# Kernel optimization log

Measured on AMD Instinct MI355X. Metric: run time of the kernel, lower is better.

## Reference

```python
import jax, jax.numpy as jnp
import numpy as np

EPS = 1e-08
TOP_K_PERCENT = 0.3


def _stft_mag(x, n_fft, hop):
    # torch.stft defaults: center=True (reflect pad n_fft//2), window=None (rect), onesided
    pad = n_fft // 2
    xp = jnp.pad(x, ((0, 0), (pad, pad)), mode='reflect')
    n_frames = 1 + (xp.shape[-1] - n_fft) // hop
    idx = jnp.arange(n_frames)[:, None] * hop + jnp.arange(n_fft)[None, :]
    frames = xp[:, idx]                       # [B, T, n_fft]
    spec = jnp.fft.rfft(frames, axis=-1)      # [B, T, F]
    mag = jnp.abs(spec).swapaxes(-1, -2)      # [B, F, T]
    return jnp.maximum(mag, EPS)


def _patchify(m, ps):
    # same patch partition as torch unfold/unfold/reshape (within-patch element
    # order differs but only per-patch means are consumed)
    B, F, T = m.shape
    pf = (-F) % ps
    pt = (-T) % ps
    mp = jnp.pad(m, ((0, 0), (0, pf), (0, pt)))
    nF, nT = (F + pf) // ps, (T + pt) // ps
    return mp.reshape(B, nF, ps, nT, ps).transpose(0, 1, 3, 2, 4).reshape(B, nF * nT, ps * ps)


def setup_inputs() -> dict:
    key = jax.random.key(0)
    ks, kt, kg = jax.random.split(key, 3)
    B, L = 16, 262144
    return {
        'student_waveform': jax.random.normal(ks, (B, L), dtype=jnp.float32),
        'teacher_waveform': jax.random.normal(kt, (B, L), dtype=jnp.float32),
        'target_waveform': jax.random.normal(kg, (B, L), dtype=jnp.float32),
        'n_fft': 1024,
        'hop_length': 256,
        'patch_size': 16,
    }


def reference(student_waveform, teacher_waveform, target_waveform, n_fft, hop_length, patch_size):
    s_mag = _stft_mag(student_waveform, n_fft, hop_length)
    t_mag = _stft_mag(teacher_waveform, n_fft, hop_length)
    g_mag = _stft_mag(target_waveform, n_fft, hop_length)

    s_p = _patchify(s_mag, patch_size)   # [B, P, ps*ps]
    t_p = _patchify(t_mag, patch_size)
    g_p = _patchify(g_mag, patch_size)

    err_s = jnp.mean(jnp.abs(s_p - g_p), axis=-1)   # [B, P]
    err_t = jnp.mean(jnp.abs(t_p - g_p), axis=-1)
    kgs = err_s - err_t
    patch_loss = jnp.mean((s_p - t_p) ** 2, axis=-1)

    B, P = patch_loss.shape
    k = max(1, int(P * TOP_K_PERCENT))
    _, idx = jax.lax.top_k(kgs, k)                   # [B, k]
    mask = jnp.zeros_like(kgs).at[jnp.arange(B)[:, None], idx].set(1.0)
    selected = jnp.sum(patch_loss * mask, axis=1)
    count = jnp.maximum(jnp.sum(mask, axis=1), 1.0)
    loss = jnp.mean(selected / count)

    sel_ratio = jnp.mean(mask)
    kgs_mean = jnp.mean(kgs)
    kgs_pos_ratio = jnp.mean((kgs > 0).astype(jnp.float32))
    return loss, sel_ratio, kgs_mean, kgs_pos_ratio
```

## Files before the change

kernel.cpp:

```cpp
#include <hip/hip_runtime.h>
#include <hip/hip_bf16.h>
#include <math.h>

#define BATCH 16
#define LEN   262144
#define HOP   256
#define PADW  512
#define NFREQ 513
#define NFRM  1025
#define NPAIR 513
#define NPT   65
#define NPF   33
#define NPATCH 2145
#define TOPK  643
#define EPSV  1e-8f
#define PSTRIDE 99

#define SW(i) ((i) ^ (((i) >> 4) & 15))

__device__ __forceinline__ int reflect_idx(int g) {
    g = (g < 0) ? -g : g;
    g = (g >= LEN) ? (2 * LEN - 2 - g) : g;
    return g;
}

__device__ __forceinline__ void load_pack(float2* xs,
    const float* __restrict__ re_src, const float* __restrict__ im_src,
    int startRe, int startIm, int tid)
{
    #pragma unroll
    for (int m = 0; m < 4; ++m) {
        const int i = tid + 256 * m;
        xs[SW(i)] = make_float2(re_src[reflect_idx(startRe + i)],
                                im_src[reflect_idx(startIm + i)]);
    }
    __syncthreads();
}

__device__ __forceinline__ void fft1024(float2* xs, const float2* tw, int tid) {
    #pragma unroll
    for (int s = 0; s < 5; ++s) {
        const int lenlog = 10 - 2 * s;
        const int q      = 1 << (lenlog - 2);
        const int pos    = tid & (q - 1);
        const int blk    = tid >> (lenlog - 2);
        const int i0     = (blk << lenlog) + pos;

        float2 a  = xs[SW(i0)];
        float2 bb = xs[SW(i0 + q)];
        float2 c  = xs[SW(i0 + 2 * q)];
        float2 d  = xs[SW(i0 + 3 * q)];

        const float t0x = a.x + c.x,  t0y = a.y + c.y;
        const float t1x = a.x - c.x,  t1y = a.y - c.y;
        const float t2x = bb.x + d.x, t2y = bb.y + d.y;
        const float t3x = bb.x - d.x, t3y = bb.y - d.y;

        const float y0x = t0x + t2x, y0y = t0y + t2y;
        const float y1x = t1x + t3y, y1y = t1y - t3x;
        const float y2x = t0x - t2x, y2y = t0y - t2y;
        const float y3x = t1x - t3y, y3y = t1y + t3x;

        const int e = pos << (2 * s);
        const float2 w1 = tw[SW(e)];
        const float2 w2 = make_float2(w1.x * w1.x - w1.y * w1.y, 2.0f * w1.x * w1.y);
        const float2 w3 = make_float2(w2.x * w1.x - w2.y * w1.y, w2.x * w1.y + w2.y * w1.x);

        xs[SW(i0)]         = make_float2(y0x, y0y);
        xs[SW(i0 + q)]     = make_float2(y1x * w1.x - y1y * w1.y, y1x * w1.y + y1y * w1.x);
        xs[SW(i0 + 2 * q)] = make_float2(y2x * w2.x - y2y * w2.y, y2x * w2.y + y2y * w2.x);
        xs[SW(i0 + 3 * q)] = make_float2(y3x * w3.x - y3y * w3.y, y3x * w3.y + y3y * w3.x);
        __syncthreads();
    }
}

__device__ __forceinline__ void unpack_mags(const float2* xs,
    float* __restrict__ magA, float* __restrict__ magB, int tid)
{
    for (int k = tid; k < NFREQ; k += 256) {
        const unsigned rk = __brev((unsigned)k) >> 22;
        const unsigned pk = ((rk & 0x155u) << 1) | ((rk & 0x2AAu) >> 1);
        const unsigned mI = (unsigned)(1024 - k) & 1023u;
        const unsigned rm = __brev(mI) >> 22;
        const unsigned pm = ((rm & 0x155u) << 1) | ((rm & 0x2AAu) >> 1);
        const float2 Zk = xs[SW(pk)];
        const float2 Zm = xs[SW(pm)];
        const float ar = Zk.x + Zm.x, ai = Zk.y - Zm.y;
        const float br = Zk.y + Zm.y, bi = Zk.x - Zm.x;
        magA[k] = fmaxf(0.5f * sqrtf(ar * ar + ai * ai), EPSV);
        magB[k] = fmaxf(0.5f * sqrtf(br * br + bi * bi), EPSV);
    }
    __syncthreads();
}

__global__ __launch_bounds__(256) void stft_pair_kernel(
    const float* __restrict__ s_in, const float* __restrict__ t_in,
    const float* __restrict__ g_in,
    float* __restrict__ part)
{
    __shared__ float2 xs[1024];
    __shared__ float2 tw[256];
    __shared__ float magS[2][516];
    __shared__ float magT[2][516];
    __shared__ float magG[2][516];

    const int tid = threadIdx.x;
    const int p   = blockIdx.x;
    const int b   = blockIdx.y;

    const float* sp = s_in + (size_t)b * LEN;
    const float* tp = t_in + (size_t)b * LEN;
    const float* gp = g_in + (size_t)b * LEN;

    {
        float sv, cv;
        sincosf(-6.283185307179586476925f * (float)tid * (1.0f / 1024.0f), &sv, &cv);
        tw[SW(tid)] = make_float2(cv, sv);
    }

    const bool hasB  = (2 * p + 1) < NFRM;
    const int startA = 2 * p * HOP - PADW;
    const int startB = startA + HOP;

    load_pack(xs, sp, tp, startA, startA, tid);
    fft1024(xs, tw, tid);
    unpack_mags(xs, magS[0], magT[0], tid);

    if (hasB) {
        load_pack(xs, sp, tp, startB, startB, tid);
        fft1024(xs, tw, tid);
        unpack_mags(xs, magS[1], magT[1], tid);
    }

    load_pack(xs, gp, gp, startA, startB, tid);
    fft1024(xs, tw, tid);
    unpack_mags(xs, magG[0], magG[1], tid);

    float* prow = part + ((size_t)b * NPAIR + p) * PSTRIDE;
    #pragma unroll
    for (int it = 0; it < 3; ++it) {
        const int f = tid + 256 * it;
        float asum = 0.0f, atsum = 0.0f, sqsum = 0.0f;
        #pragma unroll
        for (int par = 0; par < 2; ++par) {
            if (par == 1 && !hasB) break;
            float sm = 0.0f, tm = 0.0f, gm = 0.0f;
            if (f < NFREQ) { sm = magS[par][f]; tm = magT[par][f]; gm = magG[par][f]; }
            float as = fabsf(sm - gm);
            float at = fabsf(tm - gm);
            float sq = (sm - tm) * (sm - tm);
            #pragma unroll
            for (int off = 8; off >= 1; off >>= 1) {
                as += __shfl_down(as, off);
                at += __shfl_down(at, off);
                sq += __shfl_down(sq, off);
            }
            asum += as; atsum += at; sqsum += sq;
        }
        if ((tid & 15) == 0 && f < NFREQ) {
            const int g16 = f >> 4;
            prow[g16 * 3 + 0] = asum;
            prow[g16 * 3 + 1] = atsum;
            prow[g16 * 3 + 2] = sqsum;
        }
    }
}

__global__ __launch_bounds__(128) void combine_kernel(
    const float* __restrict__ part,
    float* __restrict__ kgs, float* __restrict__ pl)
{
    __shared__ float sh[PSTRIDE];
    const int tid = threadIdx.x;
    const int ti  = blockIdx.x;
    const int b   = blockIdx.y;

    if (tid < PSTRIDE) {
        float acc = 0.0f;
        const int p0 = ti * 8;
        #pragma unroll
        for (int u = 0; u < 8; ++u) {
            const int p = p0 + u;
            if (p < NPAIR) acc += part[((size_t)b * NPAIR + p) * PSTRIDE + tid];
        }
        sh[tid] = acc;
    }
    __syncthreads();
    if (tid < NPF) {
        const int pt = tid * NPT + ti;
        kgs[b * NPATCH + pt] = (sh[3 * tid] - sh[3 * tid + 1]) * (1.0f / 256.0f);
        pl [b * NPATCH + pt] = sh[3 * tid + 2] * (1.0f / 256.0f);
    }
}

__global__ __launch_bounds__(256) void topk_kernel(
    const float* __restrict__ kgs,
    const float* __restrict__ pl,
    float* __restrict__ rowstats)
{
    __shared__ unsigned ukey[NPATCH];
    __shared__ float    plv[NPATCH];
    __shared__ unsigned hist[256];
    __shared__ unsigned wtot[4];
    __shared__ int      tIdx[NPATCH];
    __shared__ int      tcnt;
    __shared__ unsigned selB, selHi;
    __shared__ float    red[3][4];

    const int tid = threadIdx.x;
    const int b   = blockIdx.x;
    const float* row   = kgs + b * NPATCH;
    const float* plrow = pl  + b * NPATCH;

    float lsum = 0.0f, lpos = 0.0f;
    for (int i = tid; i < NPATCH; i += 256) {
        float v = row[i];
        lsum += v;
        lpos += (v > 0.0f) ? 1.0f : 0.0f;
        plv[i] = plrow[i];
        unsigned u = __float_as_uint(v);
        ukey[i] = (u & 0x80000000u) ? ~u : (u | 0x80000000u);
    }
    if (tid == 0) tcnt = 0;
    __syncthreads();

    unsigned prefix = 0;
    int rem = TOPK;
    #pragma unroll
    for (int pass = 0; pass < 4; ++pass) {
        const int shift = 24 - 8 * pass;
        const unsigned himask = (pass == 0) ? 0u : (0xFFFFFFFFu << (shift + 8));

        hist[tid] = 0;
        __syncthreads();
        for (int i = tid; i < NPATCH; i += 256) {
            unsigned u = ukey[i];
            if ((u & himask) == (prefix & himask))
                atomicAdd(&hist[(u >> shift) & 255u], 1u);
        }
        __syncthreads();

        const unsigned h = hist[tid];
        unsigned v = h;
        const int lane = tid & 63;
        const int w    = tid >> 6;
        #pragma unroll
        for (int off = 1; off < 64; off <<= 1) {
            unsigned tval = __shfl_down(v, off);
            if (lane + off < 64) v += tval;
        }
        if (lane == 0) wtot[w] = v;
        __syncthreads();
        unsigned addv = 0;
        for (int w2 = w + 1; w2 < 4; ++w2) addv += wtot[w2];
        v += addv;
        const unsigned hi = v - h;
        if (v >= (unsigned)rem && hi < (unsigned)rem) { selB = (unsigned)tid; selHi = hi; }
        __syncthreads();
        prefix |= (selB << shift);
        rem -= (int)selHi;
        __syncthreads();
    }

    const unsigned T = prefix;
    float ssum = 0.0f;
    for (int i = tid; i < NPATCH; i += 256) {
        unsigned u = ukey[i];
        if (u > T) {
            ssum += plv[i];
        } else if (u == T) {
            int j = atomicAdd(&tcnt, 1);
            tIdx[j] = i;
        }
    }
    __syncthreads();
    const int m = tcnt;
    if (m == rem) {
        for (int j = tid; j < m; j += 256) ssum += plv[tIdx[j]];
    } else {
        for (int j = tid; j < m; j += 256) {
            const int i = tIdx[j];
            int rank = 0;
            for (int q = 0; q < m; ++q) rank += (tIdx[q] < i) ? 1 : 0;
            if (rank < rem) ssum += plv[i];
        }
    }

    #pragma unroll
    for (int off = 32; off > 0; off >>= 1) {
        ssum += __shfl_down(ssum, off);
        lsum += __shfl_down(lsum, off);
        lpos += __shfl_down(lpos, off);
    }
    if ((tid & 63) == 0) {
        const int wv = tid >> 6;
        red[0][wv] = ssum; red[1][wv] = lsum; red[2][wv] = lpos;
    }
    __syncthreads();
    if (tid == 0) {
        rowstats[b * 3 + 0] = red[0][0] + red[0][1] + red[0][2] + red[0][3];
        rowstats[b * 3 + 1] = red[1][0] + red[1][1] + red[1][2] + red[1][3];
        rowstats[b * 3 + 2] = red[2][0] + red[2][1] + red[2][2] + red[2][3];
    }
}

__global__ __launch_bounds__(64) void final_kernel(
    const float* __restrict__ rowstats,
    float* __restrict__ out)
{
    const int tid = threadIdx.x;
    float loss = 0.0f, ks = 0.0f, pc = 0.0f;
    if (tid < BATCH) {
        loss = rowstats[tid * 3 + 0] * (1.0f / (float)TOPK);
        ks   = rowstats[tid * 3 + 1];
        pc   = rowstats[tid * 3 + 2];
    }
    #pragma unroll
    for (int off = 32; off > 0; off >>= 1) {
        loss += __shfl_down(loss, off);
        ks   += __shfl_down(ks, off);
        pc   += __shfl_down(pc, off);
    }
    if (tid == 0) {
        out[0] = loss * (1.0f / (float)BATCH);
        out[1] = (float)TOPK / (float)NPATCH;
        out[2] = ks * (1.0f / ((float)BATCH * (float)NPATCH));
        out[3] = pc * (1.0f / ((float)BATCH * (float)NPATCH));
    }
}

extern "C" void kernel_launch(void* const* d_in, const int* in_sizes, int n_in,
                              void* d_out, int out_size, void* d_ws, size_t ws_size,
                              hipStream_t stream)
{
    const float* s_in = (const float*)d_in[0];
    const float* t_in = (const float*)d_in[1];
    const float* g_in = (const float*)d_in[2];
    float* out = (float*)d_out;

    float* part = (float*)d_ws;
    float* kgs  = part + (size_t)BATCH * NPAIR * PSTRIDE;
    float* pl   = kgs + (size_t)BATCH * NPATCH;
    float* rowstats = pl + (size_t)BATCH * NPATCH;

    dim3 g1(NPAIR, BATCH);
    stft_pair_kernel<<<g1, 256, 0, stream>>>(s_in, t_in, g_in, part);

    dim3 g2(NPT, BATCH);
    combine_kernel<<<g2, 128, 0, stream>>>(part, kgs, pl);

    topk_kernel<<<BATCH, 256, 0, stream>>>(kgs, pl, rowstats);

    final_kernel<<<1, 64, 0, stream>>>(rowstats, out);
}
```

Measured before the change: 191.4 us.

## Keep STFT magnitudes in registers and fuse patch combine into top-k kernel

Each thread now keeps the student and teacher magnitudes it needs in registers instead of staging all three spectra in shared arrays. The target magnitudes are computed inside the reduction loop, which frees about 12KB of LDS per block and removes the separate unpack barrier. The partial-sum buffer is laid out per frequency group, and the combine kernel is merged into a 1024-thread top-k kernel that sums the 8 frame-pair partials itself, saving one launch and one global round trip. The catch is that only 16 blocks now do the combine reads, which could make that stage serial, and register pressure in the FFT kernel goes up.

```diff
diff --git a/kernel.cpp b/kernel.cpp
--- a/kernel.cpp
+++ b/kernel.cpp
@@ -14,7 +14,6 @@
 #define NPATCH 2145
 #define TOPK  643
 #define EPSV  1e-8f
-#define PSTRIDE 99
 
 #define SW(i) ((i) ^ (((i) >> 4) & 15))
 
@@ -74,23 +73,20 @@
     }
 }
 
-__device__ __forceinline__ void unpack_mags(const float2* xs,
-    float* __restrict__ magA, float* __restrict__ magB, int tid)
-{
-    for (int k = tid; k < NFREQ; k += 256) {
-        const unsigned rk = __brev((unsigned)k) >> 22;
-        const unsigned pk = ((rk & 0x155u) << 1) | ((rk & 0x2AAu) >> 1);
-        const unsigned mI = (unsigned)(1024 - k) & 1023u;
-        const unsigned rm = __brev(mI) >> 22;
-        const unsigned pm = ((rm & 0x155u) << 1) | ((rm & 0x2AAu) >> 1);
-        const float2 Zk = xs[SW(pk)];
-        const float2 Zm = xs[SW(pm)];
-        const float ar = Zk.x + Zm.x, ai = Zk.y - Zm.y;
-        const float br = Zk.y + Zm.y, bi = Zk.x - Zm.x;
-        magA[k] = fmaxf(0.5f * sqrtf(ar * ar + ai * ai), EPSV);
-        magB[k] = fmaxf(0.5f * sqrtf(br * br + bi * bi), EPSV);
-    }
-    __syncthreads();
+__device__ __forceinline__ void unpack_k(const float2* xs, int k,
+                                         float& mx, float& my)
+{
+    const unsigned rk = __brev((unsigned)k) >> 22;
+    const unsigned pk = ((rk & 0x155u) << 1) | ((rk & 0x2AAu) >> 1);
+    const unsigned mI = (unsigned)(1024 - k) & 1023u;
+    const unsigned rm = __brev(mI) >> 22;
+    const unsigned pm = ((rm & 0x155u) << 1) | ((rm & 0x2AAu) >> 1);
+    const float2 Zk = xs[SW(pk)];
+    const float2 Zm = xs[SW(pm)];
+    const float ar = Zk.x + Zm.x, ai = Zk.y - Zm.y;
+    const float br = Zk.y + Zm.y, bi = Zk.x - Zm.x;
+    mx = fmaxf(0.5f * sqrtf(ar * ar + ai * ai), EPSV);
+    my = fmaxf(0.5f * sqrtf(br * br + bi * bi), EPSV);
 }
 
 __global__ __launch_bounds__(256) void stft_pair_kernel(
@@ -100,9 +96,6 @@
 {
     __shared__ float2 xs[1024];
     __shared__ float2 tw[256];
-    __shared__ float magS[2][516];
-    __shared__ float magT[2][516];
-    __shared__ float magG[2][516];
 
     const int tid = threadIdx.x;
     const int p   = blockIdx.x;
@@ -122,33 +115,47 @@
     const int startA = 2 * p * HOP - PADW;
     const int startB = startA + HOP;
 
+    float sA[3] = {0, 0, 0}, tA[3] = {0, 0, 0};
+    float sB[3] = {0, 0, 0}, tB[3] = {0, 0, 0};
+
     load_pack(xs, sp, tp, startA, startA, tid);
     fft1024(xs, tw, tid);
-    unpack_mags(xs, magS[0], magT[0], tid);
+    #pragma unroll
+    for (int it = 0; it < 3; ++it) {
+        const int k = tid + 256 * it;
+        if (k <= 512) unpack_k(xs, k, sA[it], tA[it]);
+    }
+    __syncthreads();
 
     if (hasB) {
         load_pack(xs, sp, tp, startB, startB, tid);
         fft1024(xs, tw, tid);
-        unpack_mags(xs, magS[1], magT[1], tid);
+        #pragma unroll
+        for (int it = 0; it < 3; ++it) {
+            const int k = tid + 256 * it;
+            if (k <= 512) unpack_k(xs, k, sB[it], tB[it]);
+        }
+        __syncthreads();
     }
 
     load_pack(xs, gp, gp, startA, startB, tid);
     fft1024(xs, tw, tid);
-    unpack_mags(xs, magG[0], magG[1], tid);
-
-    float* prow = part + ((size_t)b * NPAIR + p) * PSTRIDE;
+
     #pragma unroll
     for (int it = 0; it < 3; ++it) {
-        const int f = tid + 256 * it;
+        const int k = tid + 256 * it;
+        const bool valid = (k <= 512);
+        float gA_ = 0.0f, gB_ = 0.0f;
+        if (valid) unpack_k(xs, k, gA_, gB_);
+
         float asum = 0.0f, atsum = 0.0f, sqsum = 0.0f;
-        #pragma unroll
-        for (int par = 0; par < 2; ++par) {
-            if (par == 1 && !hasB) break;
-            float sm = 0.0f, tm = 0.0f, gm = 0.0f;
-            if (f < NFREQ) { sm = magS[par][f]; tm = magT[par][f]; gm = magG[par][f]; }
-            float as = fabsf(sm - gm);
-            float at = fabsf(tm - gm);
-            float sq = (sm - tm) * (sm - tm);
+        {
+            float as = 0.0f, at = 0.0f, sq = 0.0f;
+            if (valid) {
+                as = fabsf(sA[it] - gA_);
+                at = fabsf(tA[it] - gA_);
+                sq = (sA[it] - tA[it]) * (sA[it] - tA[it]);
+            }
             #pragma unroll
             for (int off = 8; off >= 1; off >>= 1) {
                 as += __shfl_down(as, off);
@@ -157,45 +164,31 @@
             }
             asum += as; atsum += at; sqsum += sq;
         }
-        if ((tid & 15) == 0 && f < NFREQ) {
-            const int g16 = f >> 4;
-            prow[g16 * 3 + 0] = asum;
-            prow[g16 * 3 + 1] = atsum;
-            prow[g16 * 3 + 2] = sqsum;
-        }
-    }
-}
-
-__global__ __launch_bounds__(128) void combine_kernel(
+        if (hasB) {
+            float as = 0.0f, at = 0.0f, sq = 0.0f;
+            if (valid) {
+                as = fabsf(sB[it] - gB_);
+                at = fabsf(tB[it] - gB_);
+                sq = (sB[it] - tB[it]) * (sB[it] - tB[it]);
+            }
+            #pragma unroll
+            for (int off = 8; off >= 1; off >>= 1) {
+                as += __shfl_down(as, off);
+                at += __shfl_down(at, off);
+                sq += __shfl_down(sq, off);
+            }
+            asum += as; atsum += at; sqsum += sq;
+        }
+        if ((tid & 15) == 0 && valid) {
+            const int g16 = k >> 4;
+            float* slot = part + (((size_t)b * NPF + g16) * NPAIR + p) * 3;
+            slot[0] = asum; slot[1] = atsum; slot[2] = sqsum;
+        }
+    }
+}
+
+__global__ __launch_bounds__(1024) void topk_kernel(
     const float* __restrict__ part,
-    float* __restrict__ kgs, float* __restrict__ pl)
-{
-    __shared__ float sh[PSTRIDE];
-    const int tid = threadIdx.x;
-    const int ti  = blockIdx.x;
-    const int b   = blockIdx.y;
-
-    if (tid < PSTRIDE) {
-        float acc = 0.0f;
-        const int p0 = ti * 8;
-        #pragma unroll
-        for (int u = 0; u < 8; ++u) {
-            const int p = p0 + u;
-            if (p < NPAIR) acc += part[((size_t)b * NPAIR + p) * PSTRIDE + tid];
-        }
-        sh[tid] = acc;
-    }
-    __syncthreads();
-    if (tid < NPF) {
-        const int pt = tid * NPT + ti;
-        kgs[b * NPATCH + pt] = (sh[3 * tid] - sh[3 * tid + 1]) * (1.0f / 256.0f);
-        pl [b * NPATCH + pt] = sh[3 * tid + 2] * (1.0f / 256.0f);
-    }
-}
-
-__global__ __launch_bounds__(256) void topk_kernel(
-    const float* __restrict__ kgs,
-    const float* __restrict__ pl,
     float* __restrict__ rowstats)
 {
     __shared__ unsigned ukey[NPATCH];
@@ -205,21 +198,31 @@
     __shared__ int      tIdx[NPATCH];
     __shared__ int      tcnt;
     __shared__ unsigned selB, selHi;
-    __shared__ float    red[3][4];
+    __shared__ float    red[3][16];
 
     const int tid = threadIdx.x;
     const int b   = blockIdx.x;
-    const float* row   = kgs + b * NPATCH;
-    const float* plrow = pl  + b * NPATCH;
 
     float lsum = 0.0f, lpos = 0.0f;
-    for (int i = tid; i < NPATCH; i += 256) {
-        float v = row[i];
-        lsum += v;
-        lpos += (v > 0.0f) ? 1.0f : 0.0f;
-        plv[i] = plrow[i];
-        unsigned u = __float_as_uint(v);
-        ukey[i] = (u & 0x80000000u) ? ~u : (u | 0x80000000u);
+    for (int p2 = tid; p2 < NPATCH; p2 += 1024) {
+        const int fi = p2 / NPT;
+        const int ti = p2 - fi * NPT;
+        const float* base = part + (((size_t)b * NPF + fi) * NPAIR + ti * 8) * 3;
+        float a = 0.0f, t3 = 0.0f, q = 0.0f;
+        #pragma unroll
+        for (int u = 0; u < 8; ++u) {
+            if (ti * 8 + u < NPAIR) {
+                a  += base[u * 3 + 0];
+                t3 += base[u * 3 + 1];
+                q  += base[u * 3 + 2];
+            }
+        }
+        const float kg = (a - t3) * (1.0f / 256.0f);
+        lsum += kg;
+        lpos += (kg > 0.0f) ? 1.0f : 0.0f;
+        plv[p2] = q * (1.0f / 256.0f);
+        unsigned u32 = __float_as_uint(kg);
+        ukey[p2] = (u32 & 0x80000000u) ? ~u32 : (u32 | 0x80000000u);
     }
     if (tid == 0) tcnt = 0;
     __syncthreads();
@@ -231,31 +234,35 @@
         const int shift = 24 - 8 * pass;
         const unsigned himask = (pass == 0) ? 0u : (0xFFFFFFFFu << (shift + 8));
 
-        hist[tid] = 0;
-        __syncthreads();
-        for (int i = tid; i < NPATCH; i += 256) {
+        if (tid < 256) hist[tid] = 0;
+        __syncthreads();
+        for (int i = tid; i < NPATCH; i += 1024) {
             unsigned u = ukey[i];
             if ((u & himask) == (prefix & himask))
                 atomicAdd(&hist[(u >> shift) & 255u], 1u);
         }
         __syncthreads();
 
-        const unsigned h = hist[tid];
-        unsigned v = h;
-        const int lane = tid & 63;
-        const int w    = tid >> 6;
-        #pragma unroll
-        for (int off = 1; off < 64; off <<= 1) {
-            unsigned tval = __shfl_down(v, off);
-            if (lane + off < 64) v += tval;
-        }
-        if (lane == 0) wtot[w] = v;
-        __syncthreads();
-        unsigned addv = 0;
-        for (int w2 = w + 1; w2 < 4; ++w2) addv += wtot[w2];
-        v += addv;
-        const unsigned hi = v - h;
-        if (v >= (unsigned)rem && hi < (unsigned)rem) { selB = (unsigned)tid; selHi = hi; }
+        if (tid < 256) {
+            const unsigned h = hist[tid];
+            unsigned v = h;
+            const int lane = tid & 63;
+            const int w    = tid >> 6;
+            #pragma unroll
+            for (int off = 1; off < 64; off <<= 1) {
+                unsigned tval = __shfl_down(v, off);
+                if (lane + off < 64) v += tval;
+            }
+            if (lane == 0) wtot[w] = v;
+            __syncthreads();
+            unsigned addv = 0;
+            for (int w2 = w + 1; w2 < 4; ++w2) addv += wtot[w2];
+            v += addv;
+            const unsigned hi = v - h;
+            if (v >= (unsigned)rem && hi < (unsigned)rem) { selB = (unsigned)tid; selHi = hi; }
+        } else {
+            __syncthreads();
+        }
         __syncthreads();
         prefix |= (selB << shift);
         rem -= (int)selHi;
@@ -264,7 +271,7 @@
 
     const unsigned T = prefix;
     float ssum = 0.0f;
-    for (int i = tid; i < NPATCH; i += 256) {
+    for (int i = tid; i < NPATCH; i += 1024) {
         unsigned u = ukey[i];
         if (u > T) {
             ssum += plv[i];
@@ -276,9 +283,9 @@
     __syncthreads();
     const int m = tcnt;
     if (m == rem) {
-        for (int j = tid; j < m; j += 256) ssum += plv[tIdx[j]];
+        for (int j = tid; j < m; j += 1024) ssum += plv[tIdx[j]];
     } else {
-        for (int j = tid; j < m; j += 256) {
+        for (int j = tid; j < m; j += 1024) {
             const int i = tIdx[j];
             int rank = 0;
             for (int q = 0; q < m; ++q) rank += (tIdx[q] < i) ? 1 : 0;
@@ -298,9 +305,12 @@
     }
     __syncthreads();
     if (tid == 0) {
-        rowstats[b * 3 + 0] = red[0][0] + red[0][1] + red[0][2] + red[0][3];
-        rowstats[b * 3 + 1] = red[1][0] + red[1][1] + red[1][2] + red[1][3];
-        rowstats[b * 3 + 2] = red[2][0] + red[2][1] + red[2][2] + red[2][3];
+        float a = 0.0f, c = 0.0f, d = 0.0f;
+        #pragma unroll
+        for (int i = 0; i < 16; ++i) { a += red[0][i]; c += red[1][i]; d += red[2][i]; }
+        rowstats[b * 3 + 0] = a;
+        rowstats[b * 3 + 1] = c;
+        rowstats[b * 3 + 2] = d;
     }
 }
 
@@ -339,17 +349,12 @@
     float* out = (float*)d_out;
 
     float* part = (float*)d_ws;
-    float* kgs  = part + (size_t)BATCH * NPAIR * PSTRIDE;
-    float* pl   = kgs + (size_t)BATCH * NPATCH;
-    float* rowstats = pl + (size_t)BATCH * NPATCH;
+    float* rowstats = part + (size_t)BATCH * NPF * NPAIR * 3;
 
     dim3 g1(NPAIR, BATCH);
     stft_pair_kernel<<<g1, 256, 0, stream>>>(s_in, t_in, g_in, part);
 
-    dim3 g2(NPT, BATCH);
-    combine_kernel<<<g2, 128, 0, stream>>>(part, kgs, pl);
-
-    topk_kernel<<<BATCH, 256, 0, stream>>>(kgs, pl, rowstats);
+    topk_kernel<<<BATCH, 1024, 0, stream>>>(part, rowstats);
 
     final_kernel<<<1, 64, 0, stream>>>(rowstats, out);
 }
```

Result: faster. 186.7 us (-2.5%).
